# Kernel optimization log

Measured on AMD Instinct MI355X. Metric: run time of the kernel, lower is better.

Reference implementation:

```python
import jax, jax.numpy as jnp
import numpy as np

# Standard minigrid color mapping (module references global COLOR_TO_IDX)
COLOR_TO_IDX = {'red': 0, 'green': 1, 'blue': 2, 'purple': 3, 'yellow': 4, 'grey': 5}
AGENT_FEATURE_SIZE = 13
NUM_AGENTS_PER_COLOR = {'grey': 4, 'yellow': 4}
COLOR_ORDER = sorted(NUM_AGENTS_PER_COLOR.keys())  # ['grey', 'yellow']
FEATURE_DIM = 256
B, N = 131072, 16
INPUT_DIM = (1 + sum(NUM_AGENTS_PER_COLOR.values())) * AGENT_FEATURE_SIZE  # 117


def setup_inputs() -> dict:
    key = jax.random.key(0)
    ks = jax.random.split(key, 14)
    inp = {
        'query_position': jax.random.normal(ks[0], (B, 2), jnp.float32),
        'query_direction': jax.random.normal(ks[1], (B, 4), jnp.float32),
        'query_abilities': jax.random.normal(ks[2], (B, 2), jnp.float32),
        'query_carried': jax.random.normal(ks[3], (B, 2), jnp.float32),
        'query_status': jax.random.normal(ks[4], (B, 3), jnp.float32),
        'all_agent_positions': jax.random.normal(ks[5], (B, N, 2), jnp.float32),
        'all_agent_directions': jax.random.normal(ks[6], (B, N, 4), jnp.float32),
        'all_agent_abilities': jax.random.normal(ks[7], (B, N, 2), jnp.float32),
        'all_agent_carried': jax.random.normal(ks[8], (B, N, 2), jnp.float32),
        'all_agent_status': jax.random.normal(ks[9], (B, N, 3), jnp.float32),
        'agent_color_indices': jax.random.randint(ks[10], (B, N), 0, 6, jnp.int32),
        # fc params; W stored (in, out) so y = x @ W + b (same math as torch Linear)
        'W': jax.random.normal(ks[11], (INPUT_DIM, FEATURE_DIM), jnp.float32) / np.sqrt(INPUT_DIM),
        'b': jax.random.normal(ks[12], (FEATURE_DIM,), jnp.float32) * 0.01,
    }
    return inp


def reference(query_position, query_direction, query_abilities, query_carried,
              query_status, all_agent_positions, all_agent_directions,
              all_agent_abilities, all_agent_carried, all_agent_status,
              agent_color_indices, W, b):
    batch = query_position.shape[0]
    # (B, N, 13) per-agent features, (B, 13) query features
    F = jnp.concatenate([all_agent_positions, all_agent_directions,
                         all_agent_abilities, all_agent_carried,
                         all_agent_status], axis=-1)
    query = jnp.concatenate([query_position, query_direction, query_abilities,
                             query_carried, query_status], axis=-1)
    feats = [query]
    rows = jnp.arange(batch)[:, None]  # (B, 1) for batched scatter
    for color in COLOR_ORDER:
        cidx = COLOR_TO_IDX[color]
        M = NUM_AGENTS_PER_COLOR[color]
        mask = agent_color_indices == cidx                 # (B, N)
        rank = jnp.cumsum(mask, axis=1) - 1                # slot of each matching agent
        valid = mask & (rank < M)
        slot = jnp.where(valid, rank, M)                   # dump overflow/non-match into slot M
        out = jnp.zeros((batch, M + 1, AGENT_FEATURE_SIZE), F.dtype)
        out = out.at[rows, slot].set(F)                    # unique (b, slot) per valid agent
        feats.append(out[:, :M].reshape(batch, M * AGENT_FEATURE_SIZE))
    x = jnp.concatenate(feats, axis=1)                     # (B, 117)
    return jax.nn.relu(x @ W + b)
```

## Files before the change

kernel.cpp:

```cpp
#include <hip/hip_runtime.h>


#define TM 128
#define XS_LD 136
#define THREADS 512
#define NCOL 256
#define KDIM 117

typedef short short8 __attribute__((ext_vector_type(8)));
typedef float f32x4 __attribute__((ext_vector_type(4)));

__device__ __forceinline__ short f2bf(float x) {
    unsigned u = __builtin_bit_cast(unsigned, x);
    unsigned r = (u + 0x7fffu + ((u >> 16) & 1u)) >> 16;
    return (short)r;
}

__device__ __forceinline__ void write_agent(short* xrow, int dst,
                                            const float* pos, const float* dir,
                                            const float* abil, const float* carr,
                                            const float* stat, size_t a) {
    const float2 p  = ((const float2*)pos)[a];
    const float4 d  = ((const float4*)dir)[a];
    const float2 ab = ((const float2*)abil)[a];
    const float2 ca = ((const float2*)carr)[a];
    const float* st = stat + a * 3;
    xrow[dst + 0]  = f2bf(p.x);
    xrow[dst + 1]  = f2bf(p.y);
    xrow[dst + 2]  = f2bf(d.x);
    xrow[dst + 3]  = f2bf(d.y);
    xrow[dst + 4]  = f2bf(d.z);
    xrow[dst + 5]  = f2bf(d.w);
    xrow[dst + 6]  = f2bf(ab.x);
    xrow[dst + 7]  = f2bf(ab.y);
    xrow[dst + 8]  = f2bf(ca.x);
    xrow[dst + 9]  = f2bf(ca.y);
    xrow[dst + 10] = f2bf(st[0]);
    xrow[dst + 11] = f2bf(st[1]);
    xrow[dst + 12] = f2bf(st[2]);
}

__global__ __launch_bounds__(THREADS, 2)
void mga_encoder_kernel(const float* __restrict__ qpos, const float* __restrict__ qdir,
                        const float* __restrict__ qabil, const float* __restrict__ qcarr,
                        const float* __restrict__ qstat,
                        const float* __restrict__ apos, const float* __restrict__ adir,
                        const float* __restrict__ aabil, const float* __restrict__ acarr,
                        const float* __restrict__ astat,
                        const int* __restrict__ cidx,
                        const float* __restrict__ W, const float* __restrict__ bvec,
                        float* __restrict__ out) {
    __shared__ __align__(16) short Xs[TM * XS_LD];

    const int tid  = threadIdx.x;
    const int wave = tid >> 6;
    const int lane = tid & 63;
    const int ln   = lane & 15;
    const int q    = lane >> 4;
    const int row0 = blockIdx.x * TM;

    const int r0w = (wave & 1) * 64;
    const int c0  = (wave >> 1) * 64;

    short8 bfr[4][4];
    #pragma unroll
    for (int kt = 0; kt < 4; kt++) {
        #pragma unroll
        for (int ct = 0; ct < 4; ct++) {
            short8 f;
            #pragma unroll
            for (int j = 0; j < 8; j++) {
                int k = kt * 32 + q * 8 + j;
                float wv = (k < KDIM) ? W[(size_t)k * NCOL + c0 + ct * 16 + ln] : 0.f;
                f[j] = f2bf(wv);
            }
            bfr[kt][ct] = f;
        }
    }
    float bv[4];
    #pragma unroll
    for (int ct = 0; ct < 4; ct++) bv[ct] = bvec[c0 + ct * 16 + ln];

    {
        unsigned* z = (unsigned*)Xs;
        #pragma unroll
        for (int i = 0; i < 17; i++) z[tid + THREADS * i] = 0u;
    }
    __syncthreads();

    {
        const int sub = tid & 3;
        const int r   = tid >> 2;
        const size_t b = (size_t)(row0 + r);
        short* xrow = &Xs[r * XS_LD];
        if (sub == 0) {
            const float2 qp = ((const float2*)qpos)[b];
            const float4 qd = ((const float4*)qdir)[b];
            const float2 qa = ((const float2*)qabil)[b];
            const float2 qc = ((const float2*)qcarr)[b];
            const float* qs = qstat + b * 3;
            xrow[0]  = f2bf(qp.x);  xrow[1]  = f2bf(qp.y);
            xrow[2]  = f2bf(qd.x);  xrow[3]  = f2bf(qd.y);
            xrow[4]  = f2bf(qd.z);  xrow[5]  = f2bf(qd.w);
            xrow[6]  = f2bf(qa.x);  xrow[7]  = f2bf(qa.y);
            xrow[8]  = f2bf(qc.x);  xrow[9]  = f2bf(qc.y);
            xrow[10] = f2bf(qs[0]); xrow[11] = f2bf(qs[1]); xrow[12] = f2bf(qs[2]);
        } else if (sub == 1 || sub == 2) {
            const int want = (sub == 1) ? 5 : 4;
            const int base = (sub == 1) ? 13 : 65;
            const int4* ip = (const int4*)(cidx + b * 16);
            int4 a0 = ip[0], a1 = ip[1], a2 = ip[2], a3 = ip[3];
            int c[16] = {a0.x, a0.y, a0.z, a0.w, a1.x, a1.y, a1.z, a1.w,
                         a2.x, a2.y, a2.z, a2.w, a3.x, a3.y, a3.z, a3.w};
            int cnt = 0;
            #pragma unroll
            for (int j = 0; j < 16; j++) {
                if (c[j] == want && cnt < 4) {
                    write_agent(xrow, base + cnt * 13, apos, adir, aabil, acarr, astat,
                                b * 16 + (size_t)j);
                    cnt++;
                }
            }
        }
    }
    __syncthreads();

    f32x4 acc[4][4];
    #pragma unroll
    for (int rt = 0; rt < 4; rt++)
        #pragma unroll
        for (int ct = 0; ct < 4; ct++) acc[rt][ct] = (f32x4){0.f, 0.f, 0.f, 0.f};

    #pragma unroll
    for (int kt = 0; kt < 4; kt++) {
        short8 av[4];
        #pragma unroll
        for (int rt = 0; rt < 4; rt++) {
            av[rt] = *(const short8*)&Xs[(r0w + rt * 16 + ln) * XS_LD + kt * 32 + q * 8];
        }
        #pragma unroll
        for (int rt = 0; rt < 4; rt++)
            #pragma unroll
            for (int ct = 0; ct < 4; ct++)
                acc[rt][ct] = __builtin_amdgcn_mfma_f32_16x16x32_bf16(
                    av[rt], bfr[kt][ct], acc[rt][ct], 0, 0, 0);
    }

    #pragma unroll
    for (int rt = 0; rt < 4; rt++) {
        #pragma unroll
        for (int ct = 0; ct < 4; ct++) {
            #pragma unroll
            for (int i = 0; i < 4; i++) {
                int row = row0 + r0w + rt * 16 + q * 4 + i;
                int col = c0 + ct * 16 + ln;
                float v = acc[rt][ct][i] + bv[ct];
                out[(size_t)row * NCOL + col] = fmaxf(v, 0.f);
            }
        }
    }
}

extern "C" void kernel_launch(void* const* d_in, const int* in_sizes, int n_in,
                              void* d_out, int out_size, void* d_ws, size_t ws_size,
                              hipStream_t stream) {
    const float* qpos  = (const float*)d_in[0];
    const float* qdir  = (const float*)d_in[1];
    const float* qabil = (const float*)d_in[2];
    const float* qcarr = (const float*)d_in[3];
    const float* qstat = (const float*)d_in[4];
    const float* apos  = (const float*)d_in[5];
    const float* adir  = (const float*)d_in[6];
    const float* aabil = (const float*)d_in[7];
    const float* acarr = (const float*)d_in[8];
    const float* astat = (const float*)d_in[9];
    const int*   cidx  = (const int*)d_in[10];
    const float* W     = (const float*)d_in[11];
    const float* bvec  = (const float*)d_in[12];
    float* out = (float*)d_out;

    const int B = in_sizes[0] / 2;
    const int nblocks = B / TM;

    mga_encoder_kernel<<<nblocks, THREADS, 0, stream>>>(
        qpos, qdir, qabil, qcarr, qstat, apos, adir, aabil, acarr, astat,
        cidx, W, bvec, out);
}
```

Before: 290.6 us.

## Parallelize agent gather across 16 lanes per row using ballot-based ranking

Replaces the serial per-row gather, where one thread scanned all 16 agents of a row for each color, with one thread per (row, agent) pair. Each thread computes its slot by popcounting a wave ballot masked to its 16-lane row group, then loads and converts its own agent's features only if it ranks in the first four. This spreads the gather loads across all threads, giving more memory-level parallelism and coalesced color-index reads, and removes the serial dependency chain. The query row is now written by the first 128 threads. The cost is four ballots per pass and scattered 2-byte shared stores.

```diff
diff --git a/kernel.cpp b/kernel.cpp
--- a/kernel.cpp
+++ b/kernel.cpp
@@ -14,30 +14,6 @@
     unsigned u = __builtin_bit_cast(unsigned, x);
     unsigned r = (u + 0x7fffu + ((u >> 16) & 1u)) >> 16;
     return (short)r;
-}
-
-__device__ __forceinline__ void write_agent(short* xrow, int dst,
-                                            const float* pos, const float* dir,
-                                            const float* abil, const float* carr,
-                                            const float* stat, size_t a) {
-    const float2 p  = ((const float2*)pos)[a];
-    const float4 d  = ((const float4*)dir)[a];
-    const float2 ab = ((const float2*)abil)[a];
-    const float2 ca = ((const float2*)carr)[a];
-    const float* st = stat + a * 3;
-    xrow[dst + 0]  = f2bf(p.x);
-    xrow[dst + 1]  = f2bf(p.y);
-    xrow[dst + 2]  = f2bf(d.x);
-    xrow[dst + 3]  = f2bf(d.y);
-    xrow[dst + 4]  = f2bf(d.z);
-    xrow[dst + 5]  = f2bf(d.w);
-    xrow[dst + 6]  = f2bf(ab.x);
-    xrow[dst + 7]  = f2bf(ab.y);
-    xrow[dst + 8]  = f2bf(ca.x);
-    xrow[dst + 9]  = f2bf(ca.y);
-    xrow[dst + 10] = f2bf(st[0]);
-    xrow[dst + 11] = f2bf(st[1]);
-    xrow[dst + 12] = f2bf(st[2]);
 }
 
 __global__ __launch_bounds__(THREADS, 2)
@@ -89,39 +65,73 @@
     __syncthreads();
 
     {
-        const int sub = tid & 3;
-        const int r   = tid >> 2;
-        const size_t b = (size_t)(row0 + r);
-        short* xrow = &Xs[r * XS_LD];
-        if (sub == 0) {
-            const float2 qp = ((const float2*)qpos)[b];
-            const float4 qd = ((const float4*)qdir)[b];
-            const float2 qa = ((const float2*)qabil)[b];
-            const float2 qc = ((const float2*)qcarr)[b];
-            const float* qs = qstat + b * 3;
-            xrow[0]  = f2bf(qp.x);  xrow[1]  = f2bf(qp.y);
-            xrow[2]  = f2bf(qd.x);  xrow[3]  = f2bf(qd.y);
-            xrow[4]  = f2bf(qd.z);  xrow[5]  = f2bf(qd.w);
-            xrow[6]  = f2bf(qa.x);  xrow[7]  = f2bf(qa.y);
-            xrow[8]  = f2bf(qc.x);  xrow[9]  = f2bf(qc.y);
-            xrow[10] = f2bf(qs[0]); xrow[11] = f2bf(qs[1]); xrow[12] = f2bf(qs[2]);
-        } else if (sub == 1 || sub == 2) {
-            const int want = (sub == 1) ? 5 : 4;
-            const int base = (sub == 1) ? 13 : 65;
-            const int4* ip = (const int4*)(cidx + b * 16);
-            int4 a0 = ip[0], a1 = ip[1], a2 = ip[2], a3 = ip[3];
-            int c[16] = {a0.x, a0.y, a0.z, a0.w, a1.x, a1.y, a1.z, a1.w,
-                         a2.x, a2.y, a2.z, a2.w, a3.x, a3.y, a3.z, a3.w};
-            int cnt = 0;
-            #pragma unroll
-            for (int j = 0; j < 16; j++) {
-                if (c[j] == want && cnt < 4) {
-                    write_agent(xrow, base + cnt * 13, apos, adir, aabil, acarr, astat,
-                                b * 16 + (size_t)j);
-                    cnt++;
+        const int j  = tid & 15;
+        const int rr = tid >> 4;
+        const int grp = lane & 0x30;
+        const unsigned long long rowmask = 0xFFFFull << grp;
+        const unsigned long long below   = (1ull << lane) - 1ull;
+
+        int cs[4];
+        #pragma unroll
+        for (int p = 0; p < 4; p++)
+            cs[p] = cidx[((size_t)(row0 + p * 32 + rr)) * 16 + j];
+
+        #pragma unroll
+        for (int p = 0; p < 4; p++) {
+            const int r = p * 32 + rr;
+            const size_t b = (size_t)(row0 + r);
+            const int c = cs[p];
+            const bool isg = (c == 5);
+            const bool isy = (c == 4);
+            const unsigned long long bg = __ballot(isg);
+            const unsigned long long by = __ballot(isy);
+            if (isg | isy) {
+                const unsigned long long bal = isg ? bg : by;
+                const int rank = __popcll(bal & rowmask & below);
+                if (rank < 4) {
+                    const int dst = (isg ? 13 : 65) + rank * 13;
+                    short* xrow = &Xs[r * XS_LD];
+                    const size_t a = b * 16 + (size_t)j;
+                    const float2 pp  = ((const float2*)apos)[a];
+                    const float4 dd  = ((const float4*)adir)[a];
+                    const float2 ab  = ((const float2*)aabil)[a];
+                    const float2 ca  = ((const float2*)acarr)[a];
+                    const float s0 = astat[a * 3 + 0];
+                    const float s1 = astat[a * 3 + 1];
+                    const float s2 = astat[a * 3 + 2];
+                    xrow[dst + 0]  = f2bf(pp.x);
+                    xrow[dst + 1]  = f2bf(pp.y);
+                    xrow[dst + 2]  = f2bf(dd.x);
+                    xrow[dst + 3]  = f2bf(dd.y);
+                    xrow[dst + 4]  = f2bf(dd.z);
+                    xrow[dst + 5]  = f2bf(dd.w);
+                    xrow[dst + 6]  = f2bf(ab.x);
+                    xrow[dst + 7]  = f2bf(ab.y);
+                    xrow[dst + 8]  = f2bf(ca.x);
+                    xrow[dst + 9]  = f2bf(ca.y);
+                    xrow[dst + 10] = f2bf(s0);
+                    xrow[dst + 11] = f2bf(s1);
+                    xrow[dst + 12] = f2bf(s2);
                 }
             }
         }
+    }
+    if (tid < TM) {
+        const size_t b = (size_t)(row0 + tid);
+        short* xrow = &Xs[tid * XS_LD];
+        const float2 qp = ((const float2*)qpos)[b];
+        const float4 qd = ((const float4*)qdir)[b];
+        const float2 qa = ((const float2*)qabil)[b];
+        const float2 qc = ((const float2*)qcarr)[b];
+        const float s0 = qstat[b * 3 + 0];
+        const float s1 = qstat[b * 3 + 1];
+        const float s2 = qstat[b * 3 + 2];
+        xrow[0]  = f2bf(qp.x);  xrow[1]  = f2bf(qp.y);
+        xrow[2]  = f2bf(qd.x);  xrow[3]  = f2bf(qd.y);
+        xrow[4]  = f2bf(qd.z);  xrow[5]  = f2bf(qd.w);
+        xrow[6]  = f2bf(qa.x);  xrow[7]  = f2bf(qa.y);
+        xrow[8]  = f2bf(qc.x);  xrow[9]  = f2bf(qc.y);
+        xrow[10] = f2bf(s0);    xrow[11] = f2bf(s1);    xrow[12] = f2bf(s2);
     }
     __syncthreads();
 
@@ -135,9 +145,8 @@
     for (int kt = 0; kt < 4; kt++) {
         short8 av[4];
         #pragma unroll
-        for (int rt = 0; rt < 4; rt++) {
+        for (int rt = 0; rt < 4; rt++)
             av[rt] = *(const short8*)&Xs[(r0w + rt * 16 + ln) * XS_LD + kt * 32 + q * 8];
-        }
         #pragma unroll
         for (int rt = 0; rt < 4; rt++)
             #pragma unroll
```

After: 263.2 us. -9.4%, faster.
